# Optimization experiments

Hardware: AMD Instinct MI355X
Metric: run time of the kernel (lower is better)

The kernel has to match this reference:

```python
import jax, jax.numpy as jnp
import numpy as np

DIM = 2048; DEPTH = 3; NLAT = 256
HEADS = 8; DHEAD = 64; INNER = HEADS * DHEAD  # 512
T, N = 24, 49  # hardcoded group structure: 24 segments x 49 tokens
MULT = 4; EPS = 1e-5
SCALE = DHEAD ** -0.5


def ln(x, s, b):
    m = jnp.mean(x, axis=-1, keepdims=True)
    v = jnp.mean((x - m) ** 2, axis=-1, keepdims=True)
    return (x - m) * jax.lax.rsqrt(v + EPS) * s + b


def setup_inputs() -> dict:
    key = jax.random.key(0)
    ks = iter(jax.random.split(key, 32))
    def rn(shape, scale=0.02):
        return jax.random.normal(next(ks), shape, dtype=jnp.float32) * scale
    return {
        "x": jax.random.normal(next(ks), (16, T * N, DIM), dtype=jnp.float32),
        "g_norm_s": jnp.ones((DIM,), jnp.float32), "g_norm_b": jnp.zeros((DIM,), jnp.float32),
        "g_wq": rn((DIM, INNER)), "g_wkv": rn((DIM, 2 * INNER)), "g_wo": rn((INNER, DIM)),
        "seg_emb": rn((T, DIM), 1.0),
        "latents": rn((NLAT, DIM), 1.0),
        "a_nm_s": jnp.ones((DEPTH, DIM), jnp.float32), "a_nm_b": jnp.zeros((DEPTH, DIM), jnp.float32),
        "a_nl_s": jnp.ones((DEPTH, DIM), jnp.float32), "a_nl_b": jnp.zeros((DEPTH, DIM), jnp.float32),
        "a_wq": rn((DEPTH, DIM, INNER)), "a_wkv": rn((DEPTH, DIM, 2 * INNER)), "a_wo": rn((DEPTH, INNER, DIM)),
        "f_n_s": jnp.ones((DEPTH, DIM), jnp.float32), "f_n_b": jnp.zeros((DEPTH, DIM), jnp.float32),
        "f_w1": rn((DEPTH, DIM, DIM * MULT)), "f_w2": rn((DEPTH, DIM * MULT, DIM)),
        "out_n_s": jnp.ones((DIM,), jnp.float32), "out_n_b": jnp.zeros((DIM,), jnp.float32),
    }


def reference(x, g_norm_s, g_norm_b, g_wq, g_wkv, g_wo, seg_emb, latents,
              a_nm_s, a_nm_b, a_nl_s, a_nl_b, a_wq, a_wkv, a_wo,
              f_n_s, f_n_b, f_w1, f_w2, out_n_s, out_n_b):
    b = x.shape[0]

    # ---- GroupAttention: block-diagonal attention within 24 groups of 49 ----
    x1 = ln(x, g_norm_s, g_norm_b)
    q = x1 @ g_wq                                   # (b, T*N, INNER)
    k, v = jnp.split(x1 @ g_wkv, 2, axis=-1)
    def to_groups(t):  # (b, T*N, h*d) -> (b, h, T, N, d)
        return t.reshape(b, T, N, HEADS, DHEAD).transpose(0, 3, 1, 2, 4)
    qg, kg, vg = to_groups(q), to_groups(k), to_groups(v)
    sim = jnp.einsum('bhtid,bhtjd->bhtij', qg * SCALE, kg)  # (b,h,T,N,N)
    sim = sim - jax.lax.stop_gradient(jnp.max(sim, axis=-1, keepdims=True))
    attn = jax.nn.softmax(sim, axis=-1)
    out = jnp.einsum('bhtij,bhtjd->bhtid', attn, vg)
    out = out.transpose(0, 2, 3, 1, 4).reshape(b, T * N, INNER) @ g_wo

    # segment embeddings: each of 24 rows repeated over its 49 tokens
    x = out + jnp.repeat(seg_emb, N, axis=0)        # (b, T*N, DIM)

    x = x[:, None]                                   # (b, 1, T*N, DIM)
    lat = jnp.broadcast_to(latents, (b, 1, NLAT, DIM))

    for l in range(DEPTH):
        # ---- PerceiverAttention: latents attend to concat(media, latents) ----
        xm = ln(x, a_nm_s[l], a_nm_b[l])
        lm = ln(lat, a_nl_s[l], a_nl_b[l])
        q = lm @ a_wq[l]                             # (b,1,NLAT,INNER)
        kv = jnp.concatenate([xm, lm], axis=2) @ a_wkv[l]
        k, v = jnp.split(kv, 2, axis=-1)             # (b,1,T*N+NLAT,INNER)
        def heads(t):  # (b,1,n,h*d) -> (b,h,1,n,d)
            return t.reshape(b, 1, t.shape[2], HEADS, DHEAD).transpose(0, 3, 1, 2, 4)
        qh, kh, vh = heads(q), heads(k), heads(v)
        sim = jnp.einsum('bhtid,bhtjd->bhtij', qh * SCALE, kh)
        sim = sim - jax.lax.stop_gradient(jnp.max(sim, axis=-1, keepdims=True))
        attn = jax.nn.softmax(sim, axis=-1)
        o = jnp.einsum('bhtij,bhtjd->bhtid', attn, vh)
        o = o.transpose(0, 2, 3, 1, 4).reshape(b, 1, NLAT, INNER) @ a_wo[l]
        lat = lat + o
        # ---- FeedForward: LN -> Linear -> GELU(exact) -> Linear ----
        h = ln(lat, f_n_s[l], f_n_b[l]) @ f_w1[l]
        lat = lat + jax.nn.gelu(h, approximate=False) @ f_w2[l]

    return ln(lat, out_n_s, out_n_b)[:, 0]           # (b, NLAT, DIM)
```

## Files before the change

kernel.cpp:

```cpp
#include <hip/hip_runtime.h>
#include <math.h>

typedef unsigned short u16;
typedef __attribute__((ext_vector_type(8))) __bf16 bf16x8;
typedef __attribute__((ext_vector_type(4))) float f32x4;
typedef __attribute__((ext_vector_type(4))) u16 u16x4;

#define DIM    2048
#define NLAT   256
#define HEADS  8
#define DHEAD  64
#define INNER  512
#define TT     24
#define NN     49
#define SEQ    (TT*NN)
#define BATCH  16
#define MROWS  (BATCH*SEQ)
#define LROWS  (BATCH*NLAT)
#define KEYS   (SEQ+NLAT)
#define KPAD   1536
#define FF     (DIM*4)
#define SCALE  0.125f

__device__ __forceinline__ u16 f2bf(float f) {
  union { float f; unsigned u; } c; c.f = f;
  unsigned r = c.u + 0x7FFFu + ((c.u >> 16) & 1u);
  return (u16)(r >> 16);
}

#define AS1(p) ((__attribute__((address_space(1))) void*)(p))
#define AS3(p) ((__attribute__((address_space(3))) void*)(p))

__global__ __launch_bounds__(256) void transpose_bf16(
    const float* __restrict__ W, u16* __restrict__ Wt, int K, int N)
{
  __shared__ float tile[32][33];
  const int tx = threadIdx.x & 31, ty = threadIdx.x >> 5;
  const int n0 = blockIdx.x * 32, k0 = blockIdx.y * 32;
  #pragma unroll
  for (int p = 0; p < 4; ++p)
    tile[ty + p*8][tx] = W[(size_t)(k0 + ty + p*8) * N + n0 + tx];
  __syncthreads();
  #pragma unroll
  for (int p = 0; p < 4; ++p)
    Wt[(size_t)(n0 + ty + p*8) * K + k0 + tx] = f2bf(tile[tx][ty + p*8]);
}

template<typename OUT>
__global__ __launch_bounds__(256) void ln_row(
    const float* __restrict__ x, const float* __restrict__ s,
    const float* __restrict__ b, OUT* __restrict__ y)
{
  const size_t row = blockIdx.x;
  const int tid = threadIdx.x;
  const f32x4* xr = (const f32x4*)(x + row * DIM);
  f32x4 v0 = xr[tid], v1 = xr[tid + 256];
  float sum = v0[0]+v0[1]+v0[2]+v0[3] + v1[0]+v1[1]+v1[2]+v1[3];
  float sq  = v0[0]*v0[0]+v0[1]*v0[1]+v0[2]*v0[2]+v0[3]*v0[3]
            + v1[0]*v1[0]+v1[1]*v1[1]+v1[2]*v1[2]+v1[3]*v1[3];
  #pragma unroll
  for (int o = 32; o > 0; o >>= 1) { sum += __shfl_down(sum, o); sq += __shfl_down(sq, o); }
  __shared__ float red[18];
  const int wave = tid >> 6, lane = tid & 63;
  if (lane == 0) { red[wave] = sum; red[8 + wave] = sq; }
  __syncthreads();
  if (tid == 0) {
    float S = red[0]+red[1]+red[2]+red[3];
    float Q = red[8]+red[9]+red[10]+red[11];
    float m = S * (1.0f/DIM);
    float var = Q * (1.0f/DIM) - m*m;
    red[16] = m; red[17] = rsqrtf(var + 1e-5f);
  }
  __syncthreads();
  const float m = red[16], inv = red[17];
  const f32x4* s4 = (const f32x4*)s; const f32x4* b4 = (const f32x4*)b;
  f32x4 o0 = (v0 - m) * inv * s4[tid]       + b4[tid];
  f32x4 o1 = (v1 - m) * inv * s4[tid + 256] + b4[tid + 256];
  if (sizeof(OUT) == 2) {
    u16x4 a = {f2bf(o0[0]), f2bf(o0[1]), f2bf(o0[2]), f2bf(o0[3])};
    u16x4 c = {f2bf(o1[0]), f2bf(o1[1]), f2bf(o1[2]), f2bf(o1[3])};
    u16x4* yr = (u16x4*)((u16*)y + row * DIM);
    yr[tid] = a; yr[tid + 256] = c;
  } else {
    f32x4* yr = (f32x4*)((float*)y + row * DIM);
    yr[tid] = o0; yr[tid + 256] = o1;
  }
}

template<int EPI>
__global__ __launch_bounds__(256) void gemm_bf16(
    const u16* __restrict__ A, const u16* __restrict__ Bt, void* __restrict__ Cv,
    const float* __restrict__ res, const float* __restrict__ seg,
    int M, int N, int K)
{
  __shared__ u16 lA[128 * 32];
  __shared__ u16 lB[128 * 32];
  const int tid  = threadIdx.x;
  const int wave = tid >> 6, lane = tid & 63;
  const int rowBase = blockIdx.y * 128, colBase = blockIdx.x * 128;
  const int wr = (wave >> 1) * 64, wc = (wave & 1) * 64;
  const int quad = lane >> 4, l16 = lane & 15;
  const int srow = lane >> 2, chunk = lane & 3;

  f32x4 acc[4][4] = {};

  for (int k0 = 0; k0 < K; k0 += 32) {
    #pragma unroll
    for (int c = 0; c < 2; ++c) {
      const int seg16 = wave * 2 + c;
      const int row = seg16 * 16 + srow;
      const u16* gA = A  + (size_t)(rowBase + row) * K + k0 + chunk * 8;
      const u16* gB = Bt + (size_t)(colBase + row) * K + k0 + chunk * 8;
      __builtin_amdgcn_global_load_lds(AS1(gA), AS3(&lA[seg16 * 512]), 16, 0, 0);
      __builtin_amdgcn_global_load_lds(AS1(gB), AS3(&lB[seg16 * 512]), 16, 0, 0);
    }
    __syncthreads();
    bf16x8 af[4], bf[4];
    #pragma unroll
    for (int i = 0; i < 4; ++i)
      af[i] = *(const bf16x8*)&lA[(wr + i*16 + l16) * 32 + quad * 8];
    #pragma unroll
    for (int j = 0; j < 4; ++j)
      bf[j] = *(const bf16x8*)&lB[(wc + j*16 + l16) * 32 + quad * 8];
    #pragma unroll
    for (int i = 0; i < 4; ++i)
      #pragma unroll
      for (int j = 0; j < 4; ++j)
        acc[i][j] = __builtin_amdgcn_mfma_f32_16x16x32_bf16(af[i], bf[j], acc[i][j], 0, 0, 0);
    __syncthreads();
  }

  #pragma unroll
  for (int i = 0; i < 4; ++i) {
    #pragma unroll
    for (int j = 0; j < 4; ++j) {
      const int col = colBase + wc + j*16 + l16;
      #pragma unroll
      for (int r = 0; r < 4; ++r) {
        const int row = rowBase + wr + i*16 + quad*4 + r;
        const size_t idx = (size_t)row * N + col;
        float val = acc[i][j][r];
        if (EPI == 0) {
          ((float*)Cv)[idx] = val;
        } else if (EPI == 1) {
          const int t = (row % SEQ) / NN;
          ((float*)Cv)[idx] = val + seg[t * DIM + col];
        } else if (EPI == 2) {
          ((float*)Cv)[idx] = val + res[idx];
        } else if (EPI == 3) {
          float g = 0.5f * val * (1.0f + erff(val * 0.70710678118f));
          ((u16*)Cv)[idx] = f2bf(g);
        } else {
          ((u16*)Cv)[idx] = f2bf(val);
        }
      }
    }
  }
}

__global__ __launch_bounds__(512) void attn_local(
    const float* __restrict__ Q, const float* __restrict__ KV, u16* __restrict__ out)
{
  const int b = blockIdx.x / TT, t = blockIdx.x % TT;
  const int h = threadIdx.x >> 6, qi = threadIdx.x & 63;
  if (qi >= NN) return;
  const size_t rowq = (size_t)b * SEQ + t * NN + qi;
  const f32x4* qr = (const f32x4*)(Q + rowq * INNER + h * DHEAD);
  f32x4 qv[16];
  #pragma unroll
  for (int d = 0; d < 16; ++d) qv[d] = qr[d] * SCALE;
  f32x4 ov[16] = {};
  float l = 0.f;
  const float* kvbase = KV + ((size_t)b * SEQ + t * NN) * 1024 + h * DHEAD;
  for (int j = 0; j < NN; ++j) {
    const f32x4* kr = (const f32x4*)(kvbase + (size_t)j * 1024);
    const f32x4* vr = (const f32x4*)(kvbase + (size_t)j * 1024 + INNER);
    float s = 0.f;
    #pragma unroll
    for (int d = 0; d < 16; ++d) {
      f32x4 k4 = kr[d];
      s += qv[d][0]*k4[0] + qv[d][1]*k4[1] + qv[d][2]*k4[2] + qv[d][3]*k4[3];
    }
    float e = __expf(s);
    l += e;
    #pragma unroll
    for (int d = 0; d < 16; ++d) ov[d] += e * vr[d];
  }
  const float rl = 1.0f / l;
  u16* orow = out + rowq * INNER + h * DHEAD;
  #pragma unroll
  for (int d = 0; d < 16; ++d) {
    f32x4 o = ov[d] * rl;
    u16x4 u = {f2bf(o[0]), f2bf(o[1]), f2bf(o[2]), f2bf(o[3])};
    *(u16x4*)(orow + d * 4) = u;
  }
}

__global__ __launch_bounds__(256) void egemm(
    const u16* __restrict__ QB, const u16* __restrict__ KVXB,
    const u16* __restrict__ KVLB, u16* __restrict__ E)
{
  __shared__ u16 lA[128 * 32];
  __shared__ u16 lB[128 * 32];
  const int tid = threadIdx.x;
  const int wave = tid >> 6, lane = tid & 63;
  const int quad = lane >> 4, l16 = lane & 15;
  const int srow = lane >> 2, chunk = lane & 3;
  const int ntile = blockIdx.x, mtile = blockIdx.y, bh = blockIdx.z;
  const int b = bh >> 3, h = bh & 7;
  const int wr = (wave >> 1) * 64, wc = (wave & 1) * 64;

  f32x4 acc[4][4] = {};

  for (int k0 = 0; k0 < DHEAD; k0 += 32) {
    #pragma unroll
    for (int c = 0; c < 2; ++c) {
      const int s = wave * 2 + c;
      const int r = s * 16 + srow;
      const u16* gA = QB + ((size_t)b * NLAT + mtile * 128 + r) * INNER
                         + h * DHEAD + k0 + chunk * 8;
      const int key = min(ntile * 128 + r, KEYS - 1);
      const u16* gB = (key < SEQ)
        ? KVXB + ((size_t)b * SEQ + key) * 1024 + h * DHEAD + k0 + chunk * 8
        : KVLB + ((size_t)b * NLAT + (key - SEQ)) * 1024 + h * DHEAD + k0 + chunk * 8;
      __builtin_amdgcn_global_load_lds(AS1(gA), AS3(&lA[s * 512]), 16, 0, 0);
      __builtin_amdgcn_global_load_lds(AS1(gB), AS3(&lB[s * 512]), 16, 0, 0);
    }
    __syncthreads();
    bf16x8 af[4], bfg[4];
    #pragma unroll
    for (int i = 0; i < 4; ++i)
      af[i] = *(const bf16x8*)&lA[(wr + i*16 + l16) * 32 + quad * 8];
    #pragma unroll
    for (int j = 0; j < 4; ++j)
      bfg[j] = *(const bf16x8*)&lB[(wc + j*16 + l16) * 32 + quad * 8];
    #pragma unroll
    for (int i = 0; i < 4; ++i)
      #pragma unroll
      for (int j = 0; j < 4; ++j)
        acc[i][j] = __builtin_amdgcn_mfma_f32_16x16x32_bf16(af[i], bfg[j], acc[i][j], 0, 0, 0);
    __syncthreads();
  }

  u16* Eb = E + ((size_t)bh * NLAT + mtile * 128) * KPAD;
  #pragma unroll
  for (int i = 0; i < 4; ++i) {
    #pragma unroll
    for (int j = 0; j < 4; ++j) {
      const int col = ntile * 128 + wc + j*16 + l16;
      #pragma unroll
      for (int r = 0; r < 4; ++r) {
        const int row = wr + i*16 + quad*4 + r;
        const float v = acc[i][j][r] * SCALE;
        Eb[(size_t)row * KPAD + col] = (col < KEYS) ? f2bf(__expf(v)) : (u16)0;
      }
    }
  }
}

__global__ __launch_bounds__(256) void vt_build(
    const u16* __restrict__ KVXB, const u16* __restrict__ KVLB, u16* __restrict__ VT)
{
  __shared__ u16 tile[32][33];
  const int tx = threadIdx.x & 31, ty = threadIdx.x >> 5;
  const int kt = blockIdx.x, dt = blockIdx.y, bh = blockIdx.z;
  const int b = bh >> 3, h = bh & 7;
  #pragma unroll
  for (int p = 0; p < 4; ++p) {
    const int key = kt * 32 + ty + p * 8;
    const int dim = dt * 32 + tx;
    u16 v = 0;
    if (key < KEYS) {
      const u16* src = (key < SEQ)
        ? KVXB + ((size_t)b * SEQ + key) * 1024 + INNER + h * DHEAD + dim
        : KVLB + ((size_t)b * NLAT + (key - SEQ)) * 1024 + INNER + h * DHEAD + dim;
      v = *src;
    }
    tile[ty + p * 8][tx] = v;
  }
  __syncthreads();
  #pragma unroll
  for (int p = 0; p < 4; ++p) {
    const int dim = dt * 32 + ty + p * 8;
    const int key = kt * 32 + tx;
    VT[((size_t)bh * DHEAD + dim) * KPAD + key] = tile[tx][ty + p * 8];
  }
}

__global__ __launch_bounds__(256) void ogemm(
    const u16* __restrict__ E, const u16* __restrict__ VT, u16* __restrict__ out)
{
  __shared__ u16 lA[128 * 32];
  __shared__ u16 lB[64 * 32];
  const int tid = threadIdx.x;
  const int wave = tid >> 6, lane = tid & 63;
  const int quad = lane >> 4, l16 = lane & 15;
  const int srow = lane >> 2, chunk = lane & 3;
  const int mtile = blockIdx.x & 1, bh = blockIdx.x >> 1;
  const int b = bh >> 3, h = bh & 7;

  const u16* Eb = E + ((size_t)bh * NLAT + mtile * 128) * KPAD;
  const u16* Vb = VT + (size_t)bh * DHEAD * KPAD;

  f32x4 acc[2][4] = {};
  f32x4 lsum[2] = {};
  bf16x8 ones;
  #pragma unroll
  for (int z = 0; z < 8; ++z) ones[z] = (__bf16)1.0f;

  for (int k0 = 0; k0 < KPAD; k0 += 32) {
    #pragma unroll
    for (int c = 0; c < 2; ++c) {
      const int s = wave * 2 + c;
      const int r = s * 16 + srow;
      const u16* gA = Eb + (size_t)r * KPAD + k0 + chunk * 8;
      __builtin_amdgcn_global_load_lds(AS1(gA), AS3(&lA[s * 512]), 16, 0, 0);
    }
    {
      const int r = wave * 16 + srow;
      const u16* gB = Vb + (size_t)r * KPAD + k0 + chunk * 8;
      __builtin_amdgcn_global_load_lds(AS1(gB), AS3(&lB[wave * 512]), 16, 0, 0);
    }
    __syncthreads();
    bf16x8 af[2], bfg[4];
    #pragma unroll
    for (int i = 0; i < 2; ++i)
      af[i] = *(const bf16x8*)&lA[(wave*32 + i*16 + l16) * 32 + quad * 8];
    #pragma unroll
    for (int j = 0; j < 4; ++j)
      bfg[j] = *(const bf16x8*)&lB[(j*16 + l16) * 32 + quad * 8];
    #pragma unroll
    for (int i = 0; i < 2; ++i) {
      lsum[i] = __builtin_amdgcn_mfma_f32_16x16x32_bf16(af[i], ones, lsum[i], 0, 0, 0);
      #pragma unroll
      for (int j = 0; j < 4; ++j)
        acc[i][j] = __builtin_amdgcn_mfma_f32_16x16x32_bf16(af[i], bfg[j], acc[i][j], 0, 0, 0);
    }
    __syncthreads();
  }

  #pragma unroll
  for (int i = 0; i < 2; ++i) {
    #pragma unroll
    for (int r = 0; r < 4; ++r) {
      const int row = mtile * 128 + wave * 32 + i * 16 + quad * 4 + r;
      const float rl = 1.0f / lsum[i][r];
      #pragma unroll
      for (int j = 0; j < 4; ++j) {
        const int col = j * 16 + l16;
        out[((size_t)b * NLAT + row) * INNER + h * DHEAD + col] = f2bf(acc[i][j][r] * rl);
      }
    }
  }
}

__global__ __launch_bounds__(256) void lat_init(
    const float* __restrict__ latents, float* __restrict__ lat)
{
  const size_t i = (size_t)blockIdx.x * 256 + threadIdx.x;
  const size_t row = i >> 9, c4 = i & 511;
  ((f32x4*)lat)[i] = ((const f32x4*)latents)[(row & (NLAT - 1)) * 512 + c4];
}

extern "C" void kernel_launch(void* const* d_in, const int* in_sizes, int n_in,
                              void* d_out, int out_size, void* d_ws, size_t ws_size,
                              hipStream_t stream) {
  const float* x        = (const float*)d_in[0];
  const float* g_norm_s = (const float*)d_in[1];
  const float* g_norm_b = (const float*)d_in[2];
  const float* g_wq     = (const float*)d_in[3];
  const float* g_wkv    = (const float*)d_in[4];
  const float* g_wo     = (const float*)d_in[5];
  const float* seg_emb  = (const float*)d_in[6];
  const float* latents  = (const float*)d_in[7];
  const float* a_nm_s   = (const float*)d_in[8];
  const float* a_nm_b   = (const float*)d_in[9];
  const float* a_nl_s   = (const float*)d_in[10];
  const float* a_nl_b   = (const float*)d_in[11];
  const float* a_wq     = (const float*)d_in[12];
  const float* a_wkv    = (const float*)d_in[13];
  const float* a_wo     = (const float*)d_in[14];
  const float* f_n_s    = (const float*)d_in[15];
  const float* f_n_b    = (const float*)d_in[16];
  const float* f_w1     = (const float*)d_in[17];
  const float* f_w2     = (const float*)d_in[18];
  const float* out_n_s  = (const float*)d_in[19];
  const float* out_n_b  = (const float*)d_in[20];

  size_t off = 0;
  auto alloc = [&](size_t bytes) -> char* {
    char* p = (char*)d_ws + off;
    off += (bytes + 255) & ~(size_t)255;
    return p;
  };
  float* XBUF  = (float*)alloc((size_t)MROWS * DIM * 4);
  u16*   TBUF  = (u16*)  alloc((size_t)MROWS * DIM * 2);
  u16*   LMBUF = (u16*)  alloc((size_t)LROWS * DIM * 2);
  float* LAT   = (float*)alloc((size_t)LROWS * DIM * 4);
  u16*   AOBUF = (u16*)  alloc((size_t)MROWS * INNER * 2);
  u16*   WT    = (u16*)  alloc((size_t)37748736 * 2);
  u16*   HBUF  = (u16*)  alloc((size_t)LROWS * FF * 2);
  char*  U     = alloc((size_t)MROWS * INNER * 4 + (size_t)MROWS * 2 * INNER * 4);
  (void)ws_size; (void)n_in; (void)in_sizes; (void)out_size;

  float* QBUF = (float*)U;
  float* KVX  = (float*)(U + (size_t)MROWS * INNER * 4);
  u16* EBUF  = (u16*)U;
  u16* VT    = (u16*)(U + (size_t)128 * NLAT * KPAD * 2);
  u16* QB    = (u16*)(U + (size_t)128 * NLAT * KPAD * 2 + (size_t)128 * DHEAD * KPAD * 2);
  u16* KVXB  = (u16*)((char*)QB + (size_t)LROWS * INNER * 2);
  u16* KVLB  = (u16*)((char*)KVXB + (size_t)MROWS * 2 * INNER * 2);

  u16* WQT  = WT;
  u16* WKVT = WT + 1048576;
  u16* WOT  = WT + 3145728;
  u16* W1T  = WT + 4194304;
  u16* W2T  = WT + 20971520;

  const dim3 b256(256);

  transpose_bf16<<<dim3(INNER/32, DIM/32), b256, 0, stream>>>(g_wq,  WQT,  DIM, INNER);
  transpose_bf16<<<dim3(2*INNER/32, DIM/32), b256, 0, stream>>>(g_wkv, WKVT, DIM, 2*INNER);
  transpose_bf16<<<dim3(DIM/32, INNER/32), b256, 0, stream>>>(g_wo,  WOT,  INNER, DIM);
  ln_row<u16><<<MROWS, b256, 0, stream>>>(x, g_norm_s, g_norm_b, TBUF);
  gemm_bf16<0><<<dim3(INNER/128, MROWS/128), b256, 0, stream>>>(TBUF, WQT, QBUF, nullptr, nullptr, MROWS, INNER, DIM);
  gemm_bf16<0><<<dim3(2*INNER/128, MROWS/128), b256, 0, stream>>>(TBUF, WKVT, KVX, nullptr, nullptr, MROWS, 2*INNER, DIM);
  attn_local<<<BATCH*TT, dim3(512), 0, stream>>>(QBUF, KVX, AOBUF);
  gemm_bf16<1><<<dim3(DIM/128, MROWS/128), b256, 0, stream>>>(AOBUF, WOT, XBUF, nullptr, seg_emb, MROWS, DIM, INNER);
  lat_init<<<(LROWS*DIM/4)/256, b256, 0, stream>>>(latents, LAT);

  for (int l = 0; l < 3; ++l) {
    transpose_bf16<<<dim3(INNER/32, DIM/32), b256, 0, stream>>>(a_wq + (size_t)l*DIM*INNER, WQT, DIM, INNER);
    transpose_bf16<<<dim3(2*INNER/32, DIM/32), b256, 0, stream>>>(a_wkv + (size_t)l*DIM*2*INNER, WKVT, DIM, 2*INNER);
    transpose_bf16<<<dim3(DIM/32, INNER/32), b256, 0, stream>>>(a_wo + (size_t)l*INNER*DIM, WOT, INNER, DIM);
    transpose_bf16<<<dim3(FF/32, DIM/32), b256, 0, stream>>>(f_w1 + (size_t)l*DIM*FF, W1T, DIM, FF);
    transpose_bf16<<<dim3(DIM/32, FF/32), b256, 0, stream>>>(f_w2 + (size_t)l*FF*DIM, W2T, FF, DIM);

    ln_row<u16><<<MROWS, b256, 0, stream>>>(XBUF, a_nm_s + l*DIM, a_nm_b + l*DIM, TBUF);
    ln_row<u16><<<LROWS, b256, 0, stream>>>(LAT, a_nl_s + l*DIM, a_nl_b + l*DIM, LMBUF);

    gemm_bf16<4><<<dim3(INNER/128, LROWS/128), b256, 0, stream>>>(LMBUF, WQT, QB, nullptr, nullptr, LROWS, INNER, DIM);
    gemm_bf16<4><<<dim3(2*INNER/128, MROWS/128), b256, 0, stream>>>(TBUF, WKVT, KVXB, nullptr, nullptr, MROWS, 2*INNER, DIM);
    gemm_bf16<4><<<dim3(2*INNER/128, LROWS/128), b256, 0, stream>>>(LMBUF, WKVT, KVLB, nullptr, nullptr, LROWS, 2*INNER, DIM);

    vt_build<<<dim3(KPAD/32, 2, 128), b256, 0, stream>>>(KVXB, KVLB, VT);
    egemm<<<dim3(KPAD/128, 2, 128), b256, 0, stream>>>(QB, KVXB, KVLB, EBUF);
    ogemm<<<dim3(256), b256, 0, stream>>>(EBUF, VT, AOBUF);

    gemm_bf16<2><<<dim3(DIM/128, LROWS/128), b256, 0, stream>>>(AOBUF, WOT, LAT, LAT, nullptr, LROWS, DIM, INNER);

    ln_row<u16><<<LROWS, b256, 0, stream>>>(LAT, f_n_s + l*DIM, f_n_b + l*DIM, LMBUF);
    gemm_bf16<3><<<dim3(FF/128, LROWS/128), b256, 0, stream>>>(LMBUF, W1T, HBUF, nullptr, nullptr, LROWS, FF, DIM);
    gemm_bf16<2><<<dim3(DIM/128, LROWS/128), b256, 0, stream>>>(HBUF, W2T, LAT, LAT, nullptr, LROWS, DIM, FF);
  }

  ln_row<float><<<LROWS, b256, 0, stream>>>(LAT, out_n_s, out_n_b, (float*)d_out);
}
```

Baseline: 3.671 ms.

## Rework GEMMs with K=64 swizzled LDS tiles, grouped scheduling, fused QKV and split-K FFN

Replaces the GEMM kernel with a version that uses a 64-wide K step, an XOR-swizzled LDS layout to avoid bank conflicts, and a remapped block order so neighbouring blocks share tiles in cache. Q and KV projections are fused into one GEMM by concatenating the transposed weights, for both the group stage and the latent stage, and attention kernels now read the combined layout. The second FFN GEMM is split along K into two partial sums that a separate kernel combines with the residual. These changes aim to raise MFMA throughput and cut launch count and occupancy loss on small grids, at the cost of more LDS per block and extra partial-sum traffic.

```diff
diff --git a/kernel.cpp b/kernel.cpp
--- a/kernel.cpp
+++ b/kernel.cpp
@@ -88,48 +88,66 @@
 }
 
 template<int EPI>
-__global__ __launch_bounds__(256) void gemm_bf16(
+__global__ __launch_bounds__(256) void gemm64(
     const u16* __restrict__ A, const u16* __restrict__ Bt, void* __restrict__ Cv,
     const float* __restrict__ res, const float* __restrict__ seg,
-    int M, int N, int K)
-{
-  __shared__ u16 lA[128 * 32];
-  __shared__ u16 lB[128 * 32];
+    int M, int N, int Klen, int lda, int ldb)
+{
+  __shared__ u16 lA[128 * 64];
+  __shared__ u16 lB[128 * 64];
   const int tid  = threadIdx.x;
   const int wave = tid >> 6, lane = tid & 63;
-  const int rowBase = blockIdx.y * 128, colBase = blockIdx.x * 128;
+  const int quad = lane >> 4, l16 = lane & 15;
+  const int srow = lane >> 3, chunk = lane & 7;
+  const int pchunk = chunk ^ srow;
+
+  const int nx = gridDim.x;
+  const int ny = M >> 7;
+  const int id = blockIdx.y * nx + blockIdx.x;
+  const int nseq = (nx * gridDim.y) >> 3;
+  const int W = (id & 7) * nseq + (id >> 3);
+  const int row_t = W / nx, col_t = W - row_t * nx;
+  if (row_t >= ny) return;
+  const int rowBase = row_t * 128, colBase = col_t * 128;
   const int wr = (wave >> 1) * 64, wc = (wave & 1) * 64;
-  const int quad = lane >> 4, l16 = lane & 15;
-  const int srow = lane >> 2, chunk = lane & 3;
+  const int koff = (EPI == 5) ? blockIdx.z * Klen : 0;
 
   f32x4 acc[4][4] = {};
 
-  for (int k0 = 0; k0 < K; k0 += 32) {
-    #pragma unroll
-    for (int c = 0; c < 2; ++c) {
-      const int seg16 = wave * 2 + c;
-      const int row = seg16 * 16 + srow;
-      const u16* gA = A  + (size_t)(rowBase + row) * K + k0 + chunk * 8;
-      const u16* gB = Bt + (size_t)(colBase + row) * K + k0 + chunk * 8;
-      __builtin_amdgcn_global_load_lds(AS1(gA), AS3(&lA[seg16 * 512]), 16, 0, 0);
-      __builtin_amdgcn_global_load_lds(AS1(gB), AS3(&lB[seg16 * 512]), 16, 0, 0);
-    }
-    __syncthreads();
-    bf16x8 af[4], bf[4];
-    #pragma unroll
-    for (int i = 0; i < 4; ++i)
-      af[i] = *(const bf16x8*)&lA[(wr + i*16 + l16) * 32 + quad * 8];
-    #pragma unroll
-    for (int j = 0; j < 4; ++j)
-      bf[j] = *(const bf16x8*)&lB[(wc + j*16 + l16) * 32 + quad * 8];
-    #pragma unroll
-    for (int i = 0; i < 4; ++i)
-      #pragma unroll
-      for (int j = 0; j < 4; ++j)
-        acc[i][j] = __builtin_amdgcn_mfma_f32_16x16x32_bf16(af[i], bf[j], acc[i][j], 0, 0, 0);
-    __syncthreads();
-  }
-
+  for (int k0 = 0; k0 < Klen; k0 += 64) {
+    #pragma unroll
+    for (int i = 0; i < 4; ++i) {
+      const int seg8 = wave * 4 + i;
+      const int row = seg8 * 8 + srow;
+      const u16* gA = A  + (size_t)(rowBase + row) * lda + koff + k0 + pchunk * 8;
+      const u16* gB = Bt + (size_t)(colBase + row) * ldb + koff + k0 + pchunk * 8;
+      __builtin_amdgcn_global_load_lds(AS1(gA), AS3(&lA[seg8 * 512]), 16, 0, 0);
+      __builtin_amdgcn_global_load_lds(AS1(gB), AS3(&lB[seg8 * 512]), 16, 0, 0);
+    }
+    __syncthreads();
+    #pragma unroll
+    for (int t = 0; t < 2; ++t) {
+      bf16x8 af[4], bfr[4];
+      #pragma unroll
+      for (int i = 0; i < 4; ++i) {
+        const int row = wr + i*16 + l16;
+        af[i] = *(const bf16x8*)&lA[row*64 + (((t*4 + quad) ^ (row & 7)) * 8)];
+      }
+      #pragma unroll
+      for (int j = 0; j < 4; ++j) {
+        const int row = wc + j*16 + l16;
+        bfr[j] = *(const bf16x8*)&lB[row*64 + (((t*4 + quad) ^ (row & 7)) * 8)];
+      }
+      #pragma unroll
+      for (int i = 0; i < 4; ++i)
+        #pragma unroll
+        for (int j = 0; j < 4; ++j)
+          acc[i][j] = __builtin_amdgcn_mfma_f32_16x16x32_bf16(af[i], bfr[j], acc[i][j], 0, 0, 0);
+    }
+    __syncthreads();
+  }
+
+  float* Pc = (EPI == 5) ? (float*)Cv + (size_t)blockIdx.z * ((size_t)M * N) : (float*)Cv;
   #pragma unroll
   for (int i = 0; i < 4; ++i) {
     #pragma unroll
@@ -141,40 +159,51 @@
         const size_t idx = (size_t)row * N + col;
         float val = acc[i][j][r];
         if (EPI == 0) {
-          ((float*)Cv)[idx] = val;
+          Pc[idx] = val;
         } else if (EPI == 1) {
           const int t = (row % SEQ) / NN;
-          ((float*)Cv)[idx] = val + seg[t * DIM + col];
+          Pc[idx] = val + seg[t * DIM + col];
         } else if (EPI == 2) {
-          ((float*)Cv)[idx] = val + res[idx];
+          Pc[idx] = val + res[idx];
         } else if (EPI == 3) {
           float g = 0.5f * val * (1.0f + erff(val * 0.70710678118f));
           ((u16*)Cv)[idx] = f2bf(g);
+        } else if (EPI == 4) {
+          ((u16*)Cv)[idx] = f2bf(val);
         } else {
-          ((u16*)Cv)[idx] = f2bf(val);
+          Pc[idx] = val;
         }
       }
     }
   }
 }
 
+__global__ __launch_bounds__(256) void combine_ffn(
+    const float* __restrict__ P, float* __restrict__ LAT)
+{
+  const size_t i = (size_t)blockIdx.x * 256 + threadIdx.x;
+  f32x4 a = ((const f32x4*)P)[i];
+  f32x4 b = ((const f32x4*)(P + (size_t)LROWS * DIM))[i];
+  ((f32x4*)LAT)[i] = ((f32x4*)LAT)[i] + a + b;
+}
+
 __global__ __launch_bounds__(512) void attn_local(
-    const float* __restrict__ Q, const float* __restrict__ KV, u16* __restrict__ out)
+    const float* __restrict__ QKV, u16* __restrict__ out)
 {
   const int b = blockIdx.x / TT, t = blockIdx.x % TT;
   const int h = threadIdx.x >> 6, qi = threadIdx.x & 63;
   if (qi >= NN) return;
   const size_t rowq = (size_t)b * SEQ + t * NN + qi;
-  const f32x4* qr = (const f32x4*)(Q + rowq * INNER + h * DHEAD);
+  const f32x4* qr = (const f32x4*)(QKV + rowq * 1536 + h * DHEAD);
   f32x4 qv[16];
   #pragma unroll
   for (int d = 0; d < 16; ++d) qv[d] = qr[d] * SCALE;
   f32x4 ov[16] = {};
   float l = 0.f;
-  const float* kvbase = KV + ((size_t)b * SEQ + t * NN) * 1024 + h * DHEAD;
+  const float* kvbase = QKV + ((size_t)b * SEQ + t * NN) * 1536 + h * DHEAD;
   for (int j = 0; j < NN; ++j) {
-    const f32x4* kr = (const f32x4*)(kvbase + (size_t)j * 1024);
-    const f32x4* vr = (const f32x4*)(kvbase + (size_t)j * 1024 + INNER);
+    const f32x4* kr = (const f32x4*)(kvbase + (size_t)j * 1536 + 512);
+    const f32x4* vr = (const f32x4*)(kvbase + (size_t)j * 1536 + 1024);
     float s = 0.f;
     #pragma unroll
     for (int d = 0; d < 16; ++d) {
@@ -197,8 +226,7 @@
 }
 
 __global__ __launch_bounds__(256) void egemm(
-    const u16* __restrict__ QB, const u16* __restrict__ KVXB,
-    const u16* __restrict__ KVLB, u16* __restrict__ E)
+    const u16* __restrict__ QKVL, const u16* __restrict__ KVXB, u16* __restrict__ E)
 {
   __shared__ u16 lA[128 * 32];
   __shared__ u16 lB[128 * 32];
@@ -217,12 +245,12 @@
     for (int c = 0; c < 2; ++c) {
       const int s = wave * 2 + c;
       const int r = s * 16 + srow;
-      const u16* gA = QB + ((size_t)b * NLAT + mtile * 128 + r) * INNER
-                         + h * DHEAD + k0 + chunk * 8;
+      const u16* gA = QKVL + ((size_t)b * NLAT + mtile * 128 + r) * 1536
+                           + h * DHEAD + k0 + chunk * 8;
       const int key = min(ntile * 128 + r, KEYS - 1);
       const u16* gB = (key < SEQ)
         ? KVXB + ((size_t)b * SEQ + key) * 1024 + h * DHEAD + k0 + chunk * 8
-        : KVLB + ((size_t)b * NLAT + (key - SEQ)) * 1024 + h * DHEAD + k0 + chunk * 8;
+        : QKVL + ((size_t)b * NLAT + (key - SEQ)) * 1536 + 512 + h * DHEAD + k0 + chunk * 8;
       __builtin_amdgcn_global_load_lds(AS1(gA), AS3(&lA[s * 512]), 16, 0, 0);
       __builtin_amdgcn_global_load_lds(AS1(gB), AS3(&lB[s * 512]), 16, 0, 0);
     }
@@ -259,7 +287,7 @@
 }
 
 __global__ __launch_bounds__(256) void vt_build(
-    const u16* __restrict__ KVXB, const u16* __restrict__ KVLB, u16* __restrict__ VT)
+    const u16* __restrict__ KVXB, const u16* __restrict__ QKVL, u16* __restrict__ VT)
 {
   __shared__ u16 tile[32][33];
   const int tx = threadIdx.x & 31, ty = threadIdx.x >> 5;
@@ -272,8 +300,8 @@
     u16 v = 0;
     if (key < KEYS) {
       const u16* src = (key < SEQ)
-        ? KVXB + ((size_t)b * SEQ + key) * 1024 + INNER + h * DHEAD + dim
-        : KVLB + ((size_t)b * NLAT + (key - SEQ)) * 1024 + INNER + h * DHEAD + dim;
+        ? KVXB + ((size_t)b * SEQ + key) * 1024 + 512 + h * DHEAD + dim
+        : QKVL + ((size_t)b * NLAT + (key - SEQ)) * 1536 + 1024 + h * DHEAD + dim;
       v = *src;
     }
     tile[ty + p * 8][tx] = v;
@@ -313,13 +341,13 @@
     for (int c = 0; c < 2; ++c) {
       const int s = wave * 2 + c;
       const int r = s * 16 + srow;
-      const u16* gA = Eb + (size_t)r * KPAD + k0 + chunk * 8;
-      __builtin_amdgcn_global_load_lds(AS1(gA), AS3(&lA[s * 512]), 16, 0, 0);
+      __builtin_amdgcn_global_load_lds(AS1(Eb + (size_t)r * KPAD + k0 + chunk * 8),
+                                       AS3(&lA[s * 512]), 16, 0, 0);
     }
     {
       const int r = wave * 16 + srow;
-      const u16* gB = Vb + (size_t)r * KPAD + k0 + chunk * 8;
-      __builtin_amdgcn_global_load_lds(AS1(gB), AS3(&lB[wave * 512]), 16, 0, 0);
+      __builtin_amdgcn_global_load_lds(AS1(Vb + (size_t)r * KPAD + k0 + chunk * 8),
+                                       AS3(&lB[wave * 512]), 16, 0, 0);
     }
     __syncthreads();
     bf16x8 af[2], bfg[4];
@@ -400,37 +428,36 @@
   u16*   AOBUF = (u16*)  alloc((size_t)MROWS * INNER * 2);
   u16*   WT    = (u16*)  alloc((size_t)37748736 * 2);
   u16*   HBUF  = (u16*)  alloc((size_t)LROWS * FF * 2);
-  char*  U     = alloc((size_t)MROWS * INNER * 4 + (size_t)MROWS * 2 * INNER * 4);
+  char*  U     = alloc((size_t)178000000);
   (void)ws_size; (void)n_in; (void)in_sizes; (void)out_size;
 
-  float* QBUF = (float*)U;
-  float* KVX  = (float*)(U + (size_t)MROWS * INNER * 4);
+  float* QKV = (float*)U;
   u16* EBUF  = (u16*)U;
+  float* PART = (float*)U;
   u16* VT    = (u16*)(U + (size_t)128 * NLAT * KPAD * 2);
-  u16* QB    = (u16*)(U + (size_t)128 * NLAT * KPAD * 2 + (size_t)128 * DHEAD * KPAD * 2);
-  u16* KVXB  = (u16*)((char*)QB + (size_t)LROWS * INNER * 2);
-  u16* KVLB  = (u16*)((char*)KVXB + (size_t)MROWS * 2 * INNER * 2);
-
-  u16* WQT  = WT;
-  u16* WKVT = WT + 1048576;
+  u16* QKVL  = (u16*)(U + (size_t)128 * NLAT * KPAD * 2 + (size_t)128 * DHEAD * KPAD * 2);
+  u16* KVXB  = (u16*)((char*)QKVL + (size_t)LROWS * 1536 * 2);
+
+  u16* Wcat = WT;
+  u16* WKVT = WT + (size_t)512 * 2048;
   u16* WOT  = WT + 3145728;
   u16* W1T  = WT + 4194304;
   u16* W2T  = WT + 20971520;
 
   const dim3 b256(256);
-
-  transpose_bf16<<<dim3(INNER/32, DIM/32), b256, 0, stream>>>(g_wq,  WQT,  DIM, INNER);
+  auto ypad = [](int nx, int ny) { while ((nx * ny) & 7) ny++; return ny; };
+
+  transpose_bf16<<<dim3(INNER/32, DIM/32), b256, 0, stream>>>(g_wq,  Wcat, DIM, INNER);
   transpose_bf16<<<dim3(2*INNER/32, DIM/32), b256, 0, stream>>>(g_wkv, WKVT, DIM, 2*INNER);
   transpose_bf16<<<dim3(DIM/32, INNER/32), b256, 0, stream>>>(g_wo,  WOT,  INNER, DIM);
   ln_row<u16><<<MROWS, b256, 0, stream>>>(x, g_norm_s, g_norm_b, TBUF);
-  gemm_bf16<0><<<dim3(INNER/128, MROWS/128), b256, 0, stream>>>(TBUF, WQT, QBUF, nullptr, nullptr, MROWS, INNER, DIM);
-  gemm_bf16<0><<<dim3(2*INNER/128, MROWS/128), b256, 0, stream>>>(TBUF, WKVT, KVX, nullptr, nullptr, MROWS, 2*INNER, DIM);
-  attn_local<<<BATCH*TT, dim3(512), 0, stream>>>(QBUF, KVX, AOBUF);
-  gemm_bf16<1><<<dim3(DIM/128, MROWS/128), b256, 0, stream>>>(AOBUF, WOT, XBUF, nullptr, seg_emb, MROWS, DIM, INNER);
+  gemm64<0><<<dim3(12, ypad(12, 147)), b256, 0, stream>>>(TBUF, Wcat, QKV, nullptr, nullptr, MROWS, 1536, DIM, DIM, DIM);
+  attn_local<<<BATCH*TT, dim3(512), 0, stream>>>(QKV, AOBUF);
+  gemm64<1><<<dim3(16, 147), b256, 0, stream>>>(AOBUF, WOT, XBUF, nullptr, seg_emb, MROWS, DIM, INNER, INNER, INNER);
   lat_init<<<(LROWS*DIM/4)/256, b256, 0, stream>>>(latents, LAT);
 
   for (int l = 0; l < 3; ++l) {
-    transpose_bf16<<<dim3(INNER/32, DIM/32), b256, 0, stream>>>(a_wq + (size_t)l*DIM*INNER, WQT, DIM, INNER);
+    transpose_bf16<<<dim3(INNER/32, DIM/32), b256, 0, stream>>>(a_wq + (size_t)l*DIM*INNER, Wcat, DIM, INNER);
     transpose_bf16<<<dim3(2*INNER/32, DIM/32), b256, 0, stream>>>(a_wkv + (size_t)l*DIM*2*INNER, WKVT, DIM, 2*INNER);
     transpose_bf16<<<dim3(DIM/32, INNER/32), b256, 0, stream>>>(a_wo + (size_t)l*INNER*DIM, WOT, INNER, DIM);
     transpose_bf16<<<dim3(FF/32, DIM/32), b256, 0, stream>>>(f_w1 + (size_t)l*DIM*FF, W1T, DIM, FF);
@@ -439,19 +466,19 @@
     ln_row<u16><<<MROWS, b256, 0, stream>>>(XBUF, a_nm_s + l*DIM, a_nm_b + l*DIM, TBUF);
     ln_row<u16><<<LROWS, b256, 0, stream>>>(LAT, a_nl_s + l*DIM, a_nl_b + l*DIM, LMBUF);
 
-    gemm_bf16<4><<<dim3(INNER/128, LROWS/128), b256, 0, stream>>>(LMBUF, WQT, QB, nullptr, nullptr, LROWS, INNER, DIM);
-    gemm_bf16<4><<<dim3(2*INNER/128, MROWS/128), b256, 0, stream>>>(TBUF, WKVT, KVXB, nullptr, nullptr, MROWS, 2*INNER, DIM);
-    gemm_bf16<4><<<dim3(2*INNER/128, LROWS/128), b256, 0, stream>>>(LMBUF, WKVT, KVLB, nullptr, nullptr, LROWS, 2*INNER, DIM);
-
-    vt_build<<<dim3(KPAD/32, 2, 128), b256, 0, stream>>>(KVXB, KVLB, VT);
-    egemm<<<dim3(KPAD/128, 2, 128), b256, 0, stream>>>(QB, KVXB, KVLB, EBUF);
+    gemm64<4><<<dim3(8, 147), b256, 0, stream>>>(TBUF, WKVT, KVXB, nullptr, nullptr, MROWS, 1024, DIM, DIM, DIM);
+    gemm64<4><<<dim3(12, 32), b256, 0, stream>>>(LMBUF, Wcat, QKVL, nullptr, nullptr, LROWS, 1536, DIM, DIM, DIM);
+
+    vt_build<<<dim3(KPAD/32, 2, 128), b256, 0, stream>>>(KVXB, QKVL, VT);
+    egemm<<<dim3(KPAD/128, 2, 128), b256, 0, stream>>>(QKVL, KVXB, EBUF);
     ogemm<<<dim3(256), b256, 0, stream>>>(EBUF, VT, AOBUF);
 
-    gemm_bf16<2><<<dim3(DIM/128, LROWS/128), b256, 0, stream>>>(AOBUF, WOT, LAT, LAT, nullptr, LROWS, DIM, INNER);
+    gemm64<2><<<dim3(16, 32), b256, 0, stream>>>(AOBUF + (size_t)0, WOT, LAT, LAT, nullptr, LROWS, DIM, INNER, INNER, INNER);
 
     ln_row<u16><<<LROWS, b256, 0, stream>>>(LAT, f_n_s + l*DIM, f_n_b + l*DIM, LMBUF);
-    gemm_bf16<3><<<dim3(FF/128, LROWS/128), b256, 0, stream>>>(LMBUF, W1T, HBUF, nullptr, nullptr, LROWS, FF, DIM);
-    gemm_bf16<2><<<dim3(DIM/128, LROWS/128), b256, 0, stream>>>(HBUF, W2T, LAT, LAT, nullptr, LROWS, DIM, FF);
+    gemm64<3><<<dim3(64, 32), b256, 0, stream>>>(LMBUF, W1T, HBUF, nullptr, nullptr, LROWS, FF, DIM, DIM, DIM);
+    gemm64<5><<<dim3(16, 32, 2), b256, 0, stream>>>(HBUF, W2T, PART, nullptr, nullptr, LROWS, DIM, FF/2, FF, FF);
+    combine_ffn<<<(LROWS*DIM/4)/256, b256, 0, stream>>>(PART, LAT);
   }
 
   ln_row<float><<<LROWS, b256, 0, stream>>>(LAT, out_n_s, out_n_b, (float*)d_out);
```

Measured after the change: 3.347 ms. 8.8% less time.
